# Optimization experiments

Hardware: AMD Instinct MI355X
Metric: run time of the kernel (lower is better)

The kernel has to match this reference:

```python
import jax, jax.numpy as jnp
import numpy as np

# ---- module constants (from init_kwargs) ----
NOF_LINKS = 64
NOISE = 1e-3          # gen_para.input_noise_power
DT = 0.01             # gen_para.dt
T_END = 5.12          # t
TXP = 1.0             # gen_para.tx_power
LAM = 1.0
RHO = 1.0

T_ARR = jnp.arange(0.0, T_END, DT, dtype=jnp.float32)   # [T] time grid
POW2T = jnp.power(jnp.float32(2.0), T_ARR)               # 2^t
POW2T_1 = POW2T - 1.0                                    # 2^t - 1
LN2 = jnp.log(jnp.float32(2.0))


def setup_inputs() -> dict:
    key = jax.random.key(0)
    k1, k2 = jax.random.split(key)
    pathloss = jax.random.uniform(k1, (NOF_LINKS, NOF_LINKS), dtype=jnp.float32)
    powers = jax.random.uniform(k2, (16, 20, NOF_LINKS), dtype=jnp.float32)
    return {"pathloss": pathloss, "powers": powers}


def _outage(pathloss, power):
    # power: [B, N, L]; pathloss: [L, L]
    B, N, L = power.shape
    T = T_ARR.shape[0]
    # signal[b,n,i,j] = pathloss[i,j] * power[b,n,i]  (per original expand/permute)
    y_ii = jnp.diagonal(pathloss)[None, None, :] * power              # [B,N,L]
    y_tot = power * jnp.sum(pathloss, axis=1)[None, None, :]          # sum_j signal
    y_ij = y_tot - y_ii
    sinr = y_ii / (y_ij + NOISE)                                      # [B,N,L]

    # block-0 outage CDF over time grid: Q1[b,i,t] = 1 - exp(-(2^t-1) * sinr[b,0,i])
    Q1 = 1.0 - jnp.exp(-POW2T_1[None, None, :] * sinr[:, 0, :, None])  # [B,L,T]

    # per-block pdf kernels for n >= 1 (vectorized over all blocks up front)
    s = sinr[:, 1:, :, None]                                          # [B,N-1,L,1]
    q = jnp.exp(-POW2T_1 * s) * POW2T * s * LN2                       # [B,N-1,L,T]

    def step(Q, qn):
        # Q, qn: [B,L,T]; per-channel grouped cross-correlation (torch conv1d semantics)
        x = Q.reshape(1, B * L, T)
        w = qn.reshape(B * L, 1, T)
        out = jax.lax.conv_general_dilated(
            x, w, window_strides=(1,), padding=[(T - 1, T - 1)],
            feature_group_count=B * L)                                 # [1,B*L,2T-1]
        Qn = out[0, :, :T].reshape(B, L, T) * DT
        return Qn, Qn[:, :, -1]

    q_scan = jnp.moveaxis(q, 1, 0)                                    # [N-1,B,L,T]
    _, outa_rest = jax.lax.scan(step, Q1, q_scan)                     # [N-1,B,L]
    outa = jnp.concatenate([Q1[None, :, :, -1], outa_rest], axis=0)   # [N,B,L]
    return jnp.moveaxis(outa, 0, 1)                                   # [B,N,L]


def reference(pathloss, powers):
    power = powers * TXP
    N = power.shape[1]
    outa = _outage(pathloss, power)                                   # [B,N,L]
    E = power[:, 0, :] + jnp.sum(power[:, 1:, :] * outa[:, :N - 1, :], axis=1)
    D = 1.0 + jnp.sum(outa[:, :N - 1, :], axis=1)
    loss = jnp.sum(E) + LAM * jnp.sum(outa[:, N - 1, :]) + RHO * jnp.sum(D)
    return loss
```

## Files before the change

### kernel.cpp

```cpp
#include <hip/hip_runtime.h>

#define LL 64
#define NN 20
#define DTC 0.01f
#define NOISEC 1e-3f
#define LN2C 0.69314718056f

typedef __attribute__((ext_vector_type(8))) short short8x;
typedef __attribute__((ext_vector_type(4))) float f32x4;

__global__ void prep_kernel(const float* __restrict__ pathloss, float* __restrict__ ws) {
    int l = threadIdx.x;
    float s = 0.f;
    #pragma unroll
    for (int j = 0; j < LL; ++j) s += pathloss[l * LL + j];
    ws[l] = s;
    ws[LL + l] = pathloss[l * LL + l];
}

__device__ __forceinline__ unsigned bf16r(float x) {
    union { float f; unsigned u; } a; a.f = x;
    return (a.u + (0x7fffu + ((a.u >> 16) & 1u))) >> 16;
}
__device__ __forceinline__ unsigned pk_bf16(float x, float y) {
    return bf16r(x) | (bf16r(y) << 16);
}

__global__ __launch_bounds__(64) void outage_kernel(
    const float* __restrict__ powers,
    const float* __restrict__ ws,
    float* __restrict__ out)
{
    __shared__ __align__(16) unsigned short gt[2][8][544];
    __shared__ __align__(16) unsigned short Qb[2][1024];

    const int lane = threadIdx.x;
    const int c = blockIdx.x, b = c >> 6, l = c & 63;
    const int nh = lane & 15;
    const int qd = lane >> 4;

    const float dg = ws[LL + l];
    const float dsum = ws[l] - dg;

    float P2[8], P1[8];
    #pragma unroll
    for (int u = 0; u < 8; ++u) {
        P2[u] = exp2f((8 * lane + u) * DTC);
        P1[u] = P2[u] - 1.f;
    }

    *((uint4*)&Qb[0][0] + lane) = uint4{0u, 0u, 0u, 0u};
    *((uint4*)&Qb[1][0] + lane) = uint4{0u, 0u, 0u, 0u};
    {
        const int bb = lane >> 5, w = lane & 31;
        #pragma unroll
        for (int k = 0; k < 8; ++k) gt[bb][k][512 + w] = 0;
    }

    const float p0 = powers[(b * NN + 0) * LL + l];
    const float s0 = dg * p0 / (p0 * dsum + NOISEC);
    float q7;
    {
        float v[8];
        #pragma unroll
        for (int u = 0; u < 8; ++u) v[u] = 1.f - expf(-P1[u] * s0);
        q7 = v[7];
        uint4 d4 = { pk_bf16(v[0], v[1]), pk_bf16(v[2], v[3]),
                     pk_bf16(v[4], v[5]), pk_bf16(v[6], v[7]) };
        *(uint4*)&Qb[0][512 + 8 * lane] = d4;
    }

    const float p1v = powers[(b * NN + 1) * LL + l];
    float lossCh = 1.f + p0 + (p1v + 1.f) * q7;

    auto fill_g = [&](int buf, float p) {
        float s  = dg * p / (p * dsum + NOISEC);
        float cm = s * LN2C * DTC;
        unsigned F[8];
        #pragma unroll
        for (int w = 0; w < 4; ++w) {
            float a  = expf(-P1[2 * w] * s) * P2[2 * w] * cm;
            float bb = expf(-P1[2 * w + 1] * s) * P2[2 * w + 1] * cm;
            F[w] = pk_bf16(a, bb);
        }
        #pragma unroll
        for (int w = 0; w < 4; ++w) {
            unsigned t = (unsigned)__shfl_down((int)F[w], 1, 64);
            F[4 + w] = (lane == 63) ? 0u : t;
        }
        unsigned E[7];
        #pragma unroll
        for (int j = 0; j < 7; ++j) E[j] = (F[j] >> 16) | (F[j + 1] << 16);
        #pragma unroll
        for (int k = 0; k < 8; ++k) {
            uint4 d4;
            if ((k & 1) == 0) d4 = uint4{F[k / 2], F[k / 2 + 1], F[k / 2 + 2], F[k / 2 + 3]};
            else              d4 = uint4{E[k / 2], E[k / 2 + 1], E[k / 2 + 2], E[k / 2 + 3]};
            *(uint4*)&gt[buf][k][8 * lane] = d4;
        }
    };
    fill_g(1, p1v);

    const int kk    = (7 - nh) & 7;
    const int baseA = 511 - nh + 8 * qd - kk;
    const int baseB = 512 + 32 * nh + 8 * qd;
    const int dstw  = 512 + 32 * nh + 4 * qd;

    for (int n = 1; n < NN; ++n) {
        const unsigned short* psrc = &Qb[(n + 1) & 1][0];
        const unsigned short* pg   = &gt[n & 1][kk][0];
        unsigned short* pdst       = &Qb[n & 1][0];

        f32x4 acc0 = {0.f, 0.f, 0.f, 0.f};
        f32x4 acc1 = {0.f, 0.f, 0.f, 0.f};
        #pragma unroll
        for (int d = 0; d < 16; ++d) {
            short8x bf = *(const short8x*)&psrc[baseB - 32 * d];
            short8x a0 = *(const short8x*)&pg[baseA - 32 * d];
            short8x a1 = *(const short8x*)&pg[baseA - 32 * d - 16];
            acc0 = __builtin_amdgcn_mfma_f32_16x16x32_bf16(a0, bf, acc0, 0, 0, 0);
            acc1 = __builtin_amdgcn_mfma_f32_16x16x32_bf16(a1, bf, acc1, 0, 0, 0);
        }

        *(uint2*)&pdst[dstw]      = uint2{pk_bf16(acc0.x, acc0.y), pk_bf16(acc0.z, acc0.w)};
        *(uint2*)&pdst[dstw + 16] = uint2{pk_bf16(acc1.x, acc1.y), pk_bf16(acc1.z, acc1.w)};

        if (n < NN - 1) {
            float pn = powers[(b * NN + n + 1) * LL + l];
            lossCh += (pn + 1.f) * acc1.w;
            fill_g((n + 1) & 1, pn);
        } else {
            lossCh += acc1.w;
        }
    }

    if (lane == 63) atomicAdd(out, lossCh);
}

extern "C" void kernel_launch(void* const* d_in, const int* in_sizes, int n_in,
                              void* d_out, int out_size, void* d_ws, size_t ws_size,
                              hipStream_t stream) {
    const float* pathloss = (const float*)d_in[0];
    const float* powers   = (const float*)d_in[1];
    float* outp = (float*)d_out;
    float* ws   = (float*)d_ws;

    (void)hipMemsetAsync(d_out, 0, sizeof(float) * out_size, stream);
    prep_kernel<<<1, 64, 0, stream>>>(pathloss, ws);
    outage_kernel<<<16 * LL, 64, 0, stream>>>(powers, ws, outp);
}
```

Before: 92.69 us.

## Fuse prep into outage kernel and overlap next-step fill with MFMA chain

Removes the separate prep kernel launch. Each block now computes its pathloss row sum and diagonal itself with wave shuffles. Inside the recurrence loop, all LDS operands are loaded into registers first, then the next step's pdf tile is written, then the MFMAs run on two independent accumulator chains. The powers value is prefetched two steps ahead. This is meant to hide LDS and global latency and shorten the dependent MFMA chain, at the cost of many more live registers (launch_bounds with one block per CU hint) and redundant per-block row sums.

New measurement: 89.80 us. -3.1%, faster.

```diff
diff --git a/kernel.cpp b/kernel.cpp
--- a/kernel.cpp
+++ b/kernel.cpp
@@ -9,15 +9,6 @@
 typedef __attribute__((ext_vector_type(8))) short short8x;
 typedef __attribute__((ext_vector_type(4))) float f32x4;
 
-__global__ void prep_kernel(const float* __restrict__ pathloss, float* __restrict__ ws) {
-    int l = threadIdx.x;
-    float s = 0.f;
-    #pragma unroll
-    for (int j = 0; j < LL; ++j) s += pathloss[l * LL + j];
-    ws[l] = s;
-    ws[LL + l] = pathloss[l * LL + l];
-}
-
 __device__ __forceinline__ unsigned bf16r(float x) {
     union { float f; unsigned u; } a; a.f = x;
     return (a.u + (0x7fffu + ((a.u >> 16) & 1u))) >> 16;
@@ -26,9 +17,9 @@
     return bf16r(x) | (bf16r(y) << 16);
 }
 
-__global__ __launch_bounds__(64) void outage_kernel(
+__global__ __launch_bounds__(64, 1) void outage_kernel(
+    const float* __restrict__ pathloss,
     const float* __restrict__ powers,
-    const float* __restrict__ ws,
     float* __restrict__ out)
 {
     __shared__ __align__(16) unsigned short gt[2][8][544];
@@ -39,8 +30,12 @@
     const int nh = lane & 15;
     const int qd = lane >> 4;
 
-    const float dg = ws[LL + l];
-    const float dsum = ws[l] - dg;
+    const float pl = pathloss[l * LL + lane];
+    float rs = pl;
+    #pragma unroll
+    for (int mk = 1; mk < 64; mk <<= 1) rs += __shfl_xor(rs, mk, 64);
+    const float dg   = __shfl(pl, l, 64);
+    const float dsum = rs - dg;
 
     float P2[8], P1[8];
     #pragma unroll
@@ -106,32 +101,44 @@
     const int baseB = 512 + 32 * nh + 8 * qd;
     const int dstw  = 512 + 32 * nh + 4 * qd;
 
+    float pnext = powers[(b * NN + 2) * LL + l];
+
     for (int n = 1; n < NN; ++n) {
         const unsigned short* psrc = &Qb[(n + 1) & 1][0];
         const unsigned short* pg   = &gt[n & 1][kk][0];
         unsigned short* pdst       = &Qb[n & 1][0];
 
-        f32x4 acc0 = {0.f, 0.f, 0.f, 0.f};
-        f32x4 acc1 = {0.f, 0.f, 0.f, 0.f};
+        float pfut = 0.f;
+        if (n <= NN - 3) pfut = powers[(b * NN + n + 2) * LL + l];
+
+        short8x Bv[16], A0v[16], A1v[16];
         #pragma unroll
         for (int d = 0; d < 16; ++d) {
-            short8x bf = *(const short8x*)&psrc[baseB - 32 * d];
-            short8x a0 = *(const short8x*)&pg[baseA - 32 * d];
-            short8x a1 = *(const short8x*)&pg[baseA - 32 * d - 16];
-            acc0 = __builtin_amdgcn_mfma_f32_16x16x32_bf16(a0, bf, acc0, 0, 0, 0);
-            acc1 = __builtin_amdgcn_mfma_f32_16x16x32_bf16(a1, bf, acc1, 0, 0, 0);
+            Bv[d]  = *(const short8x*)&psrc[baseB - 32 * d];
+            A0v[d] = *(const short8x*)&pg[baseA - 32 * d];
+            A1v[d] = *(const short8x*)&pg[baseA - 32 * d - 16];
         }
+
+        if (n < NN - 1) fill_g((n + 1) & 1, pnext);
+
+        f32x4 acc0a = {0.f, 0.f, 0.f, 0.f}, acc0b = {0.f, 0.f, 0.f, 0.f};
+        f32x4 acc1a = {0.f, 0.f, 0.f, 0.f}, acc1b = {0.f, 0.f, 0.f, 0.f};
+        #pragma unroll
+        for (int d = 0; d < 16; d += 2) {
+            acc0a = __builtin_amdgcn_mfma_f32_16x16x32_bf16(A0v[d],     Bv[d],     acc0a, 0, 0, 0);
+            acc1a = __builtin_amdgcn_mfma_f32_16x16x32_bf16(A1v[d],     Bv[d],     acc1a, 0, 0, 0);
+            acc0b = __builtin_amdgcn_mfma_f32_16x16x32_bf16(A0v[d + 1], Bv[d + 1], acc0b, 0, 0, 0);
+            acc1b = __builtin_amdgcn_mfma_f32_16x16x32_bf16(A1v[d + 1], Bv[d + 1], acc1b, 0, 0, 0);
+        }
+        f32x4 acc0 = acc0a + acc0b;
+        f32x4 acc1 = acc1a + acc1b;
 
         *(uint2*)&pdst[dstw]      = uint2{pk_bf16(acc0.x, acc0.y), pk_bf16(acc0.z, acc0.w)};
         *(uint2*)&pdst[dstw + 16] = uint2{pk_bf16(acc1.x, acc1.y), pk_bf16(acc1.z, acc1.w)};
 
-        if (n < NN - 1) {
-            float pn = powers[(b * NN + n + 1) * LL + l];
-            lossCh += (pn + 1.f) * acc1.w;
-            fill_g((n + 1) & 1, pn);
-        } else {
-            lossCh += acc1.w;
-        }
+        float wgt = (n < NN - 1) ? (pnext + 1.f) : 1.f;
+        lossCh += wgt * acc1.w;
+        pnext = pfut;
     }
 
     if (lane == 63) atomicAdd(out, lossCh);
@@ -143,9 +150,7 @@
     const float* pathloss = (const float*)d_in[0];
     const float* powers   = (const float*)d_in[1];
     float* outp = (float*)d_out;
-    float* ws   = (float*)d_ws;
 
     (void)hipMemsetAsync(d_out, 0, sizeof(float) * out_size, stream);
-    prep_kernel<<<1, 64, 0, stream>>>(pathloss, ws);
-    outage_kernel<<<16 * LL, 64, 0, stream>>>(powers, ws, outp);
+    outage_kernel<<<16 * LL, 64, 0, stream>>>(pathloss, powers, outp);
 }
```
